# Kernel tuning notes

Hardware: AMD Instinct MI355X
Metric: run time of the kernel (lower is better)

The kernel has to match this reference:

```python
import jax, jax.numpy as jnp
import numpy as np

N = 16384      # num nodes
F_IN = 128     # in_features
F_OUT = 128    # out_features


def setup_inputs() -> dict:
    key = jax.random.key(0)
    k1, k2, k3 = jax.random.split(key, 3)
    inp = jax.random.normal(k1, (N, F_IN), dtype=jnp.float32)
    adj = jax.random.uniform(k2, (N, N), dtype=jnp.float32)
    stdv = 1.0 / np.sqrt(F_OUT)
    weight = jax.random.uniform(k3, (F_IN * 2, F_OUT), dtype=jnp.float32,
                                minval=-stdv, maxval=stdv)
    return {"input": inp, "adj": adj, "weight": weight}


def reference(input, adj, weight):
    # support = adj @ input  (dense aggregation, [N, F])
    support = jnp.matmul(adj, input)
    # concat [input, support] -> [N, 2F], then transform -> [N, out]
    # Avoid materializing the concat by splitting the weight matmul:
    w_self, w_agg = weight[:F_IN], weight[F_IN:]
    return jnp.matmul(input, w_self) + jnp.matmul(support, w_agg)
```

## Files before the change

### kernel.cpp

```cpp
#include <hip/hip_runtime.h>


#define NROWS 16384
#define FDIM  128
#define NTA   64

typedef __attribute__((ext_vector_type(4))) float f32x4;
typedef __attribute__((ext_vector_type(8))) short short8;
typedef __attribute__((ext_vector_type(8))) __bf16 bf16x8;
typedef __attribute__((ext_vector_type(4))) unsigned short ushort4v;

static __device__ __forceinline__ unsigned short f2bf(float f) {
  union { __bf16 b; unsigned short u; } cvt;
  cvt.b = (__bf16)f;
  return cvt.u;
}

__global__ __launch_bounds__(256, 2)
void gcn_prep(const float* __restrict__ input, const float* __restrict__ weight,
              unsigned short* __restrict__ Yt, float* __restrict__ Z)
{
  __shared__ __align__(16) unsigned short inA[8192];
  __shared__ __align__(16) unsigned short Wt[32768];
  char* inA_c = (char*)inA;
  char* Wt_c  = (char*)Wt;

  const int tid  = threadIdx.x;
  const int lane = tid & 63;
  const int wv   = tid >> 6;
  const int m0g  = blockIdx.x * 64;

#pragma unroll
  for (int p = 0; p < 8; ++p) {
    const int idx4 = tid + p * 256;
    const int row  = idx4 >> 5;
    const int k0   = (idx4 & 31) * 4;
    const f32x4 v  = *(const f32x4*)(input + (size_t)(m0g + row) * FDIM + k0);
    ushort4v u;
#pragma unroll
    for (int i = 0; i < 4; ++i) u[i] = f2bf(v[i]);
    *(ushort4v*)(inA_c + row * 256 + ((k0 * 2) ^ ((row & 7) << 4))) = u;
  }
#pragma unroll
  for (int p = 0; p < 32; ++p) {
    const int e4   = tid + p * 256;
    const int krow = e4 >> 5;
    const int n0   = (e4 & 31) * 4;
    const f32x4 v  = *(const f32x4*)(weight + (size_t)krow * FDIM + n0);
    const int k  = krow & 127;
    const int nb = (krow >> 7) * 128;
#pragma unroll
    for (int i = 0; i < 4; ++i) {
      const int n = nb + n0 + i;
      *(unsigned short*)(Wt_c + n * 256 + ((k * 2) ^ ((n & 7) << 4))) = f2bf(v[i]);
    }
  }
  __syncthreads();

  const int rlo  = lane & 15;
  const int kgrp = lane >> 4;
  const int arow = wv * 16 + rlo;

  f32x4 acc[16];
#pragma unroll
  for (int f = 0; f < 16; ++f) acc[f] = (f32x4){0.f, 0.f, 0.f, 0.f};

#pragma unroll
  for (int s = 0; s < 4; ++s) {
    const int kb = s * 64 + kgrp * 16;
    const short8 a8 = *(const short8*)(inA_c + arow * 256 + (kb ^ ((arow & 7) << 4)));
#pragma unroll
    for (int f = 0; f < 16; ++f) {
      const int n = f * 16 + rlo;
      const short8 b8 = *(const short8*)(Wt_c + n * 256 + (kb ^ ((n & 7) << 4)));
      acc[f] = __builtin_amdgcn_mfma_f32_16x16x32_bf16(a8, b8, acc[f], 0, 0, 0);
    }
  }

  const int mg = m0g + wv * 16 + kgrp * 4;
#pragma unroll
  for (int f = 0; f < 8; ++f) {
    const int col = f * 16 + rlo;
#pragma unroll
    for (int r = 0; r < 4; ++r)
      Z[(size_t)(mg + r) * FDIM + col] = acc[f][r];
  }
  const int H = mg >> 7, ch = (mg >> 3) & 15, kin0 = mg & 7;
#pragma unroll
  for (int f = 8; f < 16; ++f) {
    const int c = f * 16 + rlo - 128;
    ushort4v u;
#pragma unroll
    for (int r = 0; r < 4; ++r) u[r] = f2bf(acc[f][r]);
    *(ushort4v*)(Yt + (size_t)H * 16384 + (size_t)(ch * 128 + c) * 8 + kin0) = u;
  }
}


#define VMCNT(n) do { asm volatile("s_waitcnt vmcnt(" #n ")" ::: "memory");        \
                      __builtin_amdgcn_sched_barrier(0); } while (0)
#define LGKM0()  do { asm volatile("s_waitcnt lgkmcnt(0)" ::: "memory");           \
                      __builtin_amdgcn_sched_barrier(0); } while (0)
#define BAR()    do { __builtin_amdgcn_s_barrier();                                \
                      __builtin_amdgcn_sched_barrier(0); } while (0)
#define SCHED()  __builtin_amdgcn_sched_barrier(0)

#define ALOAD(ka)                                                                  \
  { const char* _p = abase + (size_t)(ka) * 1024;                                  \
    asm volatile("global_load_dwordx4 %0, %1, off"            : "=v"(ar[0]) : "v"(_p)); \
    asm volatile("global_load_dwordx4 %0, %1, off offset:16"  : "=v"(ar[1]) : "v"(_p)); \
    asm volatile("global_load_dwordx4 %0, %1, off offset:256" : "=v"(ar[2]) : "v"(_p)); \
    asm volatile("global_load_dwordx4 %0, %1, off offset:272" : "=v"(ar[3]) : "v"(_p)); \
    asm volatile("global_load_dwordx4 %0, %1, off offset:512" : "=v"(ar[4]) : "v"(_p)); \
    asm volatile("global_load_dwordx4 %0, %1, off offset:528" : "=v"(ar[5]) : "v"(_p)); \
    asm volatile("global_load_dwordx4 %0, %1, off offset:768" : "=v"(ar[6]) : "v"(_p)); \
    asm volatile("global_load_dwordx4 %0, %1, off offset:784" : "=v"(ar[7]) : "v"(_p)); \
    SCHED(); }

#define ACVT_WRITE(buf)                                                            \
  { char* _aw = (char*)lds + (size_t)(buf) * 32768 + srow * 512;                   \
    _Pragma("unroll")                                                              \
    for (int _j = 0; _j < 4; ++_j) {                                               \
      bf16x8 _v;                                                                   \
      _Pragma("unroll")                                                            \
      for (int _i = 0; _i < 4; ++_i) {                                             \
        _v[_i]     = (__bf16)ar[2 * _j][_i];                                       \
        _v[_i + 4] = (__bf16)ar[2 * _j + 1][_i];                                   \
      }                                                                            \
      *(short8*)(_aw + (((_j * 8 + sj) ^ (srow & 7)) * 16)) =                      \
          __builtin_bit_cast(short8, _v);                                          \
    }                                                                              \
    SCHED(); }

#define BSTAGE(b, t)                                                               \
  { const unsigned short* _bs = Yt + (size_t)(t) * 16384;                          \
    char* _bd = (char*)lds + 65536 + (size_t)(b) * 32768;                          \
    _Pragma("unroll")                                                              \
    for (int _i = 0; _i < 4; ++_i) {                                               \
      const int _q = wv * 4 + _i;                                                  \
      __builtin_amdgcn_global_load_lds(                                            \
          (const __attribute__((address_space(1))) void*)(_bs + _q * 512 + lane * 8), \
          (__attribute__((address_space(3))) void*)(_bd + _q * 1024),              \
          16, 0, 0);                                                               \
    }                                                                              \
    SCHED(); }

#define CHALF(abuf, sub, bbuf)                                                     \
  { const char* _Ap = (const char*)lds + (size_t)(abuf) * 32768 + arow_b;          \
    const char* _Bp = (const char*)lds + 65536 + (size_t)(bbuf) * 32768;           \
    _Pragma("unroll")                                                              \
    for (int _s = 0; _s < 4; ++_s) {                                               \
      const int _c = (sub) * 16 + _s * 4 + kgrp;                                   \
      const short8 _a8 = *(const short8*)(_Ap + ((_c ^ aswz) * 16));               \
      _Pragma("unroll")                                                            \
      for (int _f = 0; _f < 4; ++_f) {                                             \
        const int _n = nh * 64 + _f * 16 + rlo;                                    \
        const short8 _b8 = *(const short8*)(_Bp + (size_t)((_s * 4 + kgrp) * 128 + _n) * 16); \
        acc[_f] = __builtin_amdgcn_mfma_f32_16x16x32_bf16(_a8, _b8, acc[_f], 0, 0, 0); \
      }                                                                            \
    } }

__global__ __launch_bounds__(512, 1)
void gcn_main(const float* __restrict__ adj, const unsigned short* __restrict__ Yt,
              const float* __restrict__ Z, float* __restrict__ out)
{
  __shared__ __align__(16) unsigned char lds[163840];

  const int tid  = threadIdx.x;
  const int lane = tid & 63;
  const int wv   = tid >> 6;
  const int rg   = wv >> 1;
  const int nh   = wv & 1;
  const int m0   = blockIdx.x * 64;
  const int rlo  = lane & 15;
  const int kgrp = lane >> 4;

  const int srow = tid >> 3;
  const int sj   = tid & 7;
  const char* abase = (const char*)(adj + (size_t)(m0 + srow) * NROWS) + sj * 32;

  const int arow_b = (rg * 16 + rlo) * 512;
  const int aswz   = rlo & 7;

  f32x4 acc[4];
#pragma unroll
  for (int f = 0; f < 4; ++f) acc[f] = (f32x4){0.f, 0.f, 0.f, 0.f};

  f32x4 ar[8];

  ALOAD(0);
  BSTAGE(0, 0);
  BSTAGE(1, 1);
  VMCNT(8);
  ACVT_WRITE(0);
  ALOAD(1);
  VMCNT(12);
  LGKM0();
  BAR();

  BSTAGE(2, 2);
  CHALF(0, 0, 0);
  VMCNT(12);
  BAR();
  BSTAGE(0, 3);
  CHALF(0, 1, 1);
  VMCNT(8);
  ACVT_WRITE(1);
  VMCNT(4);
  LGKM0();
  BAR();

  int bA = 2;
  for (int kt = 1; kt <= NTA - 2; ++kt) {
    const int abufC = kt & 1;
    const int bS0   = bA >= 1 ? bA - 1 : bA + 2;
    const int bS1   = bA;
    const int bC1   = bA < 2 ? bA + 1 : 0;
    ALOAD(kt + 1);
    BSTAGE(bS0, 2 * kt + 2);
    CHALF(abufC, 0, bA);
    VMCNT(12);
    BAR();
    BSTAGE(bS1, 2 * kt + 3);
    CHALF(abufC, 1, bC1);
    VMCNT(8);
    ACVT_WRITE(abufC ^ 1);
    VMCNT(4);
    LGKM0();
    BAR();
    bA = bS0;
  }

  CHALF(1, 0, 0);
  VMCNT(0);
  BAR();
  CHALF(1, 1, 1);

  const int rowb = m0 + rg * 16 + (lane >> 4) * 4;
#pragma unroll
  for (int f = 0; f < 4; ++f) {
    const int col = nh * 64 + f * 16 + rlo;
#pragma unroll
    for (int r = 0; r < 4; ++r) {
      const size_t idx = (size_t)(rowb + r) * FDIM + col;
      out[idx] = acc[f][r] + Z[idx];
    }
  }
}

extern "C" void kernel_launch(void* const* d_in, const int* in_sizes, int n_in,
                              void* d_out, int out_size, void* d_ws, size_t ws_size,
                              hipStream_t stream) {
  const float* input  = (const float*)d_in[0];
  const float* adj    = (const float*)d_in[1];
  const float* weight = (const float*)d_in[2];
  float* out = (float*)d_out;

  unsigned short* Yt = (unsigned short*)d_ws;
  float* Z = (float*)((char*)d_ws + (size_t)NROWS * FDIM * 2);

  gcn_prep<<<256, 256, 0, stream>>>(input, weight, Yt, Z);
  gcn_main<<<256, 512, 0, stream>>>(adj, Yt, Z, out);
}
```

Before: 220.3 us.

## Restructure adj streaming into 128-wide K tiles with dual register banks

The main GEMM loop now processes 128-column K tiles with two alternating register banks for adj loads, three rotating A and B LDS buffers, and one barrier per tile instead of two per 256-column tile. Adj loads use non-temporal hints and a new per-lane row/column mapping with an XOR-swizzled LDS write of 8-byte chunks. The goal is to keep more global loads in flight, cut LDS footprint, and reduce synchronization, at the cost of more loop iterations and smaller, possibly less efficient LDS stores.

```diff
diff --git a/kernel.cpp b/kernel.cpp
--- a/kernel.cpp
+++ b/kernel.cpp
@@ -3,7 +3,7 @@
 
 #define NROWS 16384
 #define FDIM  128
-#define NTA   64
+#define NT2   128
 
 typedef __attribute__((ext_vector_type(4))) float f32x4;
 typedef __attribute__((ext_vector_type(8))) short short8;
@@ -105,66 +105,59 @@
                       __builtin_amdgcn_sched_barrier(0); } while (0)
 #define SCHED()  __builtin_amdgcn_sched_barrier(0)
 
-#define ALOAD(ka)                                                                  \
-  { const char* _p = abase + (size_t)(ka) * 1024;                                  \
-    asm volatile("global_load_dwordx4 %0, %1, off"            : "=v"(ar[0]) : "v"(_p)); \
-    asm volatile("global_load_dwordx4 %0, %1, off offset:16"  : "=v"(ar[1]) : "v"(_p)); \
-    asm volatile("global_load_dwordx4 %0, %1, off offset:256" : "=v"(ar[2]) : "v"(_p)); \
-    asm volatile("global_load_dwordx4 %0, %1, off offset:272" : "=v"(ar[3]) : "v"(_p)); \
-    asm volatile("global_load_dwordx4 %0, %1, off offset:512" : "=v"(ar[4]) : "v"(_p)); \
-    asm volatile("global_load_dwordx4 %0, %1, off offset:528" : "=v"(ar[5]) : "v"(_p)); \
-    asm volatile("global_load_dwordx4 %0, %1, off offset:768" : "=v"(ar[6]) : "v"(_p)); \
-    asm volatile("global_load_dwordx4 %0, %1, off offset:784" : "=v"(ar[7]) : "v"(_p)); \
+#define ALOADR(BANK, ka)                                                           \
+  { const long _o = (long)(ka) * 512;                                              \
+    asm volatile("global_load_dwordx4 %0, %1, off nt" : "=v"(BANK[0]) : "v"(pA0 + _o)); \
+    asm volatile("global_load_dwordx4 %0, %1, off nt" : "=v"(BANK[1]) : "v"(pA1 + _o)); \
+    asm volatile("global_load_dwordx4 %0, %1, off nt" : "=v"(BANK[2]) : "v"(pA2 + _o)); \
+    asm volatile("global_load_dwordx4 %0, %1, off nt" : "=v"(BANK[3]) : "v"(pA3 + _o)); \
     SCHED(); }
 
-#define ACVT_WRITE(buf)                                                            \
-  { char* _aw = (char*)lds + (size_t)(buf) * 32768 + srow * 512;                   \
-    _Pragma("unroll")                                                              \
-    for (int _j = 0; _j < 4; ++_j) {                                               \
-      bf16x8 _v;                                                                   \
+#define ACVT_WRITE(BANK, aoff)                                                     \
+  { _Pragma("unroll")                                                              \
+    for (int _i = 0; _i < 4; ++_i) {                                               \
+      ushort4v _u;                                                                 \
       _Pragma("unroll")                                                            \
-      for (int _i = 0; _i < 4; ++_i) {                                             \
-        _v[_i]     = (__bf16)ar[2 * _j][_i];                                       \
-        _v[_i + 4] = (__bf16)ar[2 * _j + 1][_i];                                   \
-      }                                                                            \
-      *(short8*)(_aw + (((_j * 8 + sj) ^ (srow & 7)) * 16)) =                      \
-          __builtin_bit_cast(short8, _v);                                          \
+      for (int _j = 0; _j < 4; ++_j) _u[_j] = f2bf(BANK[_i][_j]);                  \
+      *(ushort4v*)(lds + (aoff) + awo[_i]) = _u;                                   \
     }                                                                              \
     SCHED(); }
 
-#define BSTAGE(b, t)                                                               \
+#define BSTAGE(boff, t)                                                            \
   { const unsigned short* _bs = Yt + (size_t)(t) * 16384;                          \
-    char* _bd = (char*)lds + 65536 + (size_t)(b) * 32768;                          \
     _Pragma("unroll")                                                              \
     for (int _i = 0; _i < 4; ++_i) {                                               \
       const int _q = wv * 4 + _i;                                                  \
       __builtin_amdgcn_global_load_lds(                                            \
           (const __attribute__((address_space(1))) void*)(_bs + _q * 512 + lane * 8), \
-          (__attribute__((address_space(3))) void*)(_bd + _q * 1024),              \
+          (__attribute__((address_space(3))) void*)(lds + (boff) + _q * 1024),     \
           16, 0, 0);                                                               \
     }                                                                              \
     SCHED(); }
 
-#define CHALF(abuf, sub, bbuf)                                                     \
-  { const char* _Ap = (const char*)lds + (size_t)(abuf) * 32768 + arow_b;          \
-    const char* _Bp = (const char*)lds + 65536 + (size_t)(bbuf) * 32768;           \
+#define CTILE(aoff, boff)                                                          \
+  { const char* _Ap = (const char*)lds + (aoff) + arow2;                           \
+    const char* _Bp = (const char*)lds + (boff);                                   \
     _Pragma("unroll")                                                              \
     for (int _s = 0; _s < 4; ++_s) {                                               \
-      const int _c = (sub) * 16 + _s * 4 + kgrp;                                   \
+      const int _c = _s * 4 + kgrp;                                                \
       const short8 _a8 = *(const short8*)(_Ap + ((_c ^ aswz) * 16));               \
       _Pragma("unroll")                                                            \
       for (int _f = 0; _f < 4; ++_f) {                                             \
         const int _n = nh * 64 + _f * 16 + rlo;                                    \
-        const short8 _b8 = *(const short8*)(_Bp + (size_t)((_s * 4 + kgrp) * 128 + _n) * 16); \
+        const short8 _b8 = *(const short8*)(_Bp + (size_t)(_c * 128 + _n) * 16);   \
         acc[_f] = __builtin_amdgcn_mfma_f32_16x16x32_bf16(_a8, _b8, acc[_f], 0, 0, 0); \
       }                                                                            \
     } }
+
+#define ABUF(b) ((size_t)(b) * 16384)
+#define BBUF(b) (49152 + (size_t)(b) * 32768)
 
 __global__ __launch_bounds__(512, 1)
 void gcn_main(const float* __restrict__ adj, const unsigned short* __restrict__ Yt,
               const float* __restrict__ Z, float* __restrict__ out)
 {
-  __shared__ __align__(16) unsigned char lds[163840];
+  __shared__ __align__(16) char lds[147456];
 
   const int tid  = threadIdx.x;
   const int lane = tid & 63;
@@ -175,66 +168,76 @@
   const int rlo  = lane & 15;
   const int kgrp = lane >> 4;
 
-  const int srow = tid >> 3;
-  const int sj   = tid & 7;
-  const char* abase = (const char*)(adj + (size_t)(m0 + srow) * NROWS) + sj * 32;
-
-  const int arow_b = (rg * 16 + rlo) * 512;
-  const int aswz   = rlo & 7;
+  const char* pA0;
+  const char* pA1;
+  const char* pA2;
+  const char* pA3;
+  int awo[4];
+  {
+#pragma unroll
+    for (int i = 0; i < 4; ++i) {
+      const int row_g = 2 * (wv * 4 + i) + (lane >> 5);
+      const int j     = (lane & 31) ^ (row_g & 7);
+      const char* p = (const char*)(adj + (size_t)(m0 + row_g) * NROWS + (size_t)j * 4);
+      if (i == 0) pA0 = p; else if (i == 1) pA1 = p; else if (i == 2) pA2 = p; else pA3 = p;
+      awo[i] = row_g * 256 + (((j >> 1) ^ (row_g & 7)) << 4) + ((j & 1) << 3);
+    }
+  }
+
+  const int arow2 = (rg * 16 + rlo) * 256;
+  const int aswz  = rlo & 7;
 
   f32x4 acc[4];
 #pragma unroll
   for (int f = 0; f < 4; ++f) acc[f] = (f32x4){0.f, 0.f, 0.f, 0.f};
 
-  f32x4 ar[8];
-
-  ALOAD(0);
-  BSTAGE(0, 0);
-  BSTAGE(1, 1);
+  f32x4 arA[4], arB[4];
+
+  ALOADR(arA, 0);
+  BSTAGE(BBUF(0), 0);
+  ALOADR(arB, 1);
+  BSTAGE(BBUF(1), 1);
   VMCNT(8);
-  ACVT_WRITE(0);
-  ALOAD(1);
-  VMCNT(12);
+  ACVT_WRITE(arA, ABUF(0));
   LGKM0();
   BAR();
 
-  BSTAGE(2, 2);
-  CHALF(0, 0, 0);
-  VMCNT(12);
-  BAR();
-  BSTAGE(0, 3);
-  CHALF(0, 1, 1);
-  VMCNT(8);
-  ACVT_WRITE(1);
-  VMCNT(4);
+  int bc = 0;
+  for (int tp = 0; tp < 63; ++tp) {
+    const int t0 = 2 * tp;
+    {
+      const int bs = bc == 0 ? 2 : bc - 1;
+      const int bw = bc == 2 ? 0 : bc + 1;
+      ALOADR(arA, t0 + 2);
+      BSTAGE(BBUF(bs), t0 + 2);
+      CTILE(ABUF(bc), BBUF(bc));
+      VMCNT(8);
+      ACVT_WRITE(arB, ABUF(bw));
+      LGKM0();
+      BAR();
+      bc = bw;
+    }
+    {
+      const int t1 = t0 + 1;
+      const int bs = bc == 0 ? 2 : bc - 1;
+      const int bw = bc == 2 ? 0 : bc + 1;
+      ALOADR(arB, t1 + 2);
+      BSTAGE(BBUF(bs), t1 + 2);
+      CTILE(ABUF(bc), BBUF(bc));
+      VMCNT(8);
+      ACVT_WRITE(arA, ABUF(bw));
+      LGKM0();
+      BAR();
+      bc = bw;
+    }
+  }
+
+  CTILE(ABUF(0), BBUF(0));
+  VMCNT(0);
+  ACVT_WRITE(arB, ABUF(1));
   LGKM0();
   BAR();
-
-  int bA = 2;
-  for (int kt = 1; kt <= NTA - 2; ++kt) {
-    const int abufC = kt & 1;
-    const int bS0   = bA >= 1 ? bA - 1 : bA + 2;
-    const int bS1   = bA;
-    const int bC1   = bA < 2 ? bA + 1 : 0;
-    ALOAD(kt + 1);
-    BSTAGE(bS0, 2 * kt + 2);
-    CHALF(abufC, 0, bA);
-    VMCNT(12);
-    BAR();
-    BSTAGE(bS1, 2 * kt + 3);
-    CHALF(abufC, 1, bC1);
-    VMCNT(8);
-    ACVT_WRITE(abufC ^ 1);
-    VMCNT(4);
-    LGKM0();
-    BAR();
-    bA = bS0;
-  }
-
-  CHALF(1, 0, 0);
-  VMCNT(0);
-  BAR();
-  CHALF(1, 1, 1);
+  CTILE(ABUF(1), BBUF(1));
 
   const int rowb = m0 + rg * 16 + (lane >> 4) * 4;
 #pragma unroll
```

Result: faster. 206.4 us (-6.3%).
